# Performance work log

Hardware: AMD Instinct MI355X
Metric: run time of the kernel (lower is better)

## Reference

```python
import jax, jax.numpy as jnp
import numpy as np

B, SQ, SK, D = 8, 2048, 768, 768  # SK must equal D for layer_combine concat to typecheck


def setup_inputs() -> dict:
    key = jax.random.key(0)
    ks = jax.random.split(key, 13)
    s = 0.02
    return {
        "query": jax.random.normal(ks[0], (B, SQ, D), jnp.float32),
        "key_matrix": jax.random.normal(ks[1], (B, SK, D), jnp.float32),
        "value_matrix": jax.random.normal(ks[2], (B, SK, D), jnp.float32),
        "prev_layer": jax.random.normal(ks[3], (SK, D), jnp.float32) * s,
        "attention_mask": jax.random.randint(ks[4], (B, 1, SK), 0, 2, jnp.int32),
        "Wq": jax.random.normal(ks[5], (D, D), jnp.float32) * s,
        "bq": jax.random.normal(ks[6], (D,), jnp.float32) * s,
        "Wk": jax.random.normal(ks[7], (D, D), jnp.float32) * s,
        "bk": jax.random.normal(ks[8], (D,), jnp.float32) * s,
        "Wv": jax.random.normal(ks[9], (D, D), jnp.float32) * s,
        "bv": jax.random.normal(ks[10], (D,), jnp.float32) * s,
        "Wc": jax.random.normal(ks[11], (D, 2 * D), jnp.float32) * s,
        "bc": jax.random.normal(ks[12], (D,), jnp.float32) * s,
    }


def reference(query, key_matrix, value_matrix, prev_layer, attention_mask,
              Wq, bq, Wk, bk, Wv, bv, Wc, bc):
    # Linear projections (torch Linear: x @ W.T + b)
    Q = query @ Wq.T + bq                      # [B, SQ, D]
    K = key_matrix @ Wk.T + bk                 # [B, SK, D]
    V = value_matrix @ Wv.T + bv               # computed but unused when prev_layer given (faithful)
    scale = 1.0 / np.sqrt(D).astype(np.float32)
    scores = jnp.einsum('bqd,bkd->bqk', Q, K) * scale  # [B, SQ, SK]
    scores = jnp.where(attention_mask == 0, jnp.float32(-1e9), scores)
    # prev-layer integration: matmul + concat + linear combine
    layer_attn = scores @ prev_layer           # [B, SQ, D]
    combined = jnp.concatenate([scores, layer_attn], axis=-1)  # [B, SQ, 2D]
    out = combined @ Wc.T + bc                 # [B, SQ, D]
    return out
```

## Files before the change

### kernel.cpp

```cpp
#include <hip/hip_runtime.h>
#include <hip/hip_bf16.h>


typedef __attribute__((ext_vector_type(8))) short short8;
typedef __attribute__((ext_vector_type(4))) float f32x4;

#define SCALE 0.03608439182435161f

__device__ inline unsigned short f2bf(float x) {
  unsigned int u = __builtin_bit_cast(unsigned int, x);
  u = (u + 0x7fffu + ((u >> 16) & 1u)) >> 16;
  return (unsigned short)u;
}
__device__ inline float bf2f(unsigned short h) {
  return __builtin_bit_cast(float, ((unsigned int)h) << 16);
}

__global__ void k_cvt8(const float* __restrict__ s, unsigned short* __restrict__ d, int n8) {
  int i = blockIdx.x * 256 + threadIdx.x;
  if (i >= n8) return;
  const float4* s4 = reinterpret_cast<const float4*>(s);
  float4 v0 = s4[2 * i], v1 = s4[2 * i + 1];
  ushort4* d4 = reinterpret_cast<ushort4*>(d);
  d4[2 * i]     = make_ushort4(f2bf(v0.x), f2bf(v0.y), f2bf(v0.z), f2bf(v0.w));
  d4[2 * i + 1] = make_ushort4(f2bf(v1.x), f2bf(v1.y), f2bf(v1.z), f2bf(v1.w));
}

__global__ void k_prep(const float* __restrict__ prev, const float* __restrict__ Wc,
                       unsigned short* __restrict__ prev_bf,
                       unsigned short* __restrict__ Wc2_bf) {
  int g = blockIdx.x;
  int region = g / 576;
  int idx = (g - region * 576) * 256 + threadIdx.x;
  float4 v;
  unsigned short* dst;
  if (region == 0) { v = reinterpret_cast<const float4*>(prev)[idx]; dst = prev_bf; }
  else {
    int r = idx / 192, c4 = (idx - r * 192) * 4;
    v = *reinterpret_cast<const float4*>(Wc + (long long)r * 1536 + 768 + c4);
    dst = Wc2_bf;
  }
  reinterpret_cast<ushort4*>(dst)[idx] = make_ushort4(f2bf(v.x), f2bf(v.y), f2bf(v.z), f2bf(v.w));
}

__global__ void k_tcvt(const float* __restrict__ Wq, const float* __restrict__ Wk,
                       const float* __restrict__ key, const int* __restrict__ mask,
                       unsigned short* __restrict__ WqT, unsigned short* __restrict__ WkT,
                       unsigned short* __restrict__ keyzT) {
  __shared__ float t[64][65];
  int z = blockIdx.z;
  const float* src;
  unsigned short* dst;
  const int* mb = nullptr;
  if (z == 0) { src = Wq; dst = WqT; }
  else if (z == 1) { src = Wk; dst = WkT; }
  else {
    int b = z - 2;
    src = key + (long long)b * 589824;
    dst = keyzT + (long long)b * 589824;
    mb = mask + b * 768;
  }
  int bx = blockIdx.x * 64, by = blockIdx.y * 64;
  int tx = threadIdx.x & 63, ty = threadIdx.x >> 6;
  #pragma unroll
  for (int i = 0; i < 64; i += 4) {
    float v = src[(long long)(by + ty + i) * 768 + bx + tx];
    if (mb) v = mb[by + ty + i] ? v : 0.0f;
    t[ty + i][tx] = v;
  }
  __syncthreads();
  #pragma unroll
  for (int i = 0; i < 64; i += 4)
    dst[(long long)(bx + ty + i) * 768 + by + tx] = f2bf(t[tx][ty + i]);
}

__global__ void k_sums(const unsigned short* __restrict__ WqT,
                       const unsigned short* __restrict__ WkT,
                       const float* __restrict__ bk, const float* __restrict__ bq,
                       const float* __restrict__ Mt, const int* __restrict__ mask,
                       float* __restrict__ u, float* __restrict__ w3,
                       float* __restrict__ s1, float* __restrict__ sm0) {
  int gw = blockIdx.x * 4 + (threadIdx.x >> 6);
  int lane = threadIdx.x & 63;
  if (gw < 1536) {
    const unsigned short* wrow = (gw < 768) ? (WqT + (long long)gw * 768)
                                            : (WkT + (long long)(gw - 768) * 768);
    const float* vec = (gw < 768) ? bk : bq;
    float s = 0.f;
    for (int j = lane; j < 768; j += 64) s += bf2f(wrow[j]) * vec[j];
    #pragma unroll
    for (int off = 32; off > 0; off >>= 1) s += __shfl_down(s, off, 64);
    if (lane == 0) { if (gw < 768) u[gw] = s; else w3[gw - 768] = s; }
  } else {
    int g2 = gw - 1536;
    int b = g2 / 768, d2 = g2 - b * 768;
    if (b >= 8) return;
    const int* mb = mask + b * 768;
    const float* mrow = Mt + (long long)d2 * 768;
    float a1 = 0.f, a0 = 0.f;
    for (int k = lane; k < 768; k += 64) {
      float v = mrow[k];
      if (mb[k]) a1 += v; else a0 += v;
    }
    #pragma unroll
    for (int off = 32; off > 0; off >>= 1) {
      a1 += __shfl_down(a1, off, 64);
      a0 += __shfl_down(a0, off, 64);
    }
    if (lane == 0) { s1[g2] = a1; sm0[g2] = a0; }
  }
}

__global__ void k_row(const unsigned short* __restrict__ Tt, const float* __restrict__ w3,
                      const float* __restrict__ s1, const float* __restrict__ sm0,
                      const float* __restrict__ bq, const float* __restrict__ bk,
                      const float* __restrict__ bc, float* __restrict__ row) {
  int gw = blockIdx.x * 4 + (threadIdx.x >> 6);
  int lane = threadIdx.x & 63;
  int b = gw / 768, d2 = gw - b * 768;
  if (b >= 8) return;
  const unsigned short* trow = Tt + ((long long)b * 768 + d2) * 768;
  float st = 0.f, sbb = 0.f;
  for (int j = lane; j < 768; j += 64) {
    st += bf2f(trow[j]) * w3[j];
    sbb += bq[j] * bk[j];
  }
  #pragma unroll
  for (int off = 32; off > 0; off >>= 1) {
    st += __shfl_down(st, off, 64);
    sbb += __shfl_down(sbb, off, 64);
  }
  if (lane == 0)
    row[gw] = bc[d2] - 1e9f * sm0[gw] + SCALE * (st + sbb * s1[gw]);
}

__device__ inline void xcd_swz(int& bx, int& by, int& bz) {
  const int gx = gridDim.x, gy = gridDim.y;
  const int nwg = gx * gy * (int)gridDim.z;
  int lin = blockIdx.x + gx * (blockIdx.y + gy * blockIdx.z);
  int qq = nwg >> 3, rr = nwg & 7, xcd = lin & 7, loc = lin >> 3;
  int swz = (xcd < rr ? xcd * (qq + 1) : rr * (qq + 1) + (xcd - rr) * qq) + loc;
  bz = swz / (gx * gy);
  int rem = swz - bz * gx * gy;
  by = rem / gx;
  bx = rem - by * gx;
}

__device__ inline void nt64_core(const unsigned short* Ab, int lda,
                                 const unsigned short* Bb, int ldb,
                                 int m0, int n0, int tid, f32x4 (&acc)[2][2],
                                 char* As, char* Bs) {
  const int w = tid >> 6, lane = tid & 63;
  const int wr = w >> 1, wc = w & 1;
  const int fr = lane & 15, fq = lane >> 4;
  for (int kt = 0; kt < 768; kt += 64) {
    __syncthreads();
    #pragma unroll
    for (int t = 0; t < 2; ++t) {
      int g = t * 256 + tid;
      int row = g >> 3, s = g & 7;
      int sg = (s - row) & 7;
      const unsigned short* ga = Ab + (long long)(m0 + row) * lda + kt + sg * 8;
      __builtin_amdgcn_global_load_lds(
          (const __attribute__((address_space(1))) void*)ga,
          (__attribute__((address_space(3))) void*)(As + g * 16), 16, 0, 0);
    }
    #pragma unroll
    for (int t = 0; t < 2; ++t) {
      int g = t * 256 + tid;
      int row = g >> 3, s = g & 7;
      int sg = (s - row) & 7;
      const unsigned short* gb = Bb + (long long)(n0 + row) * ldb + kt + sg * 8;
      __builtin_amdgcn_global_load_lds(
          (const __attribute__((address_space(1))) void*)gb,
          (__attribute__((address_space(3))) void*)(Bs + g * 16), 16, 0, 0);
    }
    __syncthreads();
    #pragma unroll
    for (int kk = 0; kk < 2; ++kk) {
      short8 af[2], bfr[2];
      #pragma unroll
      for (int i = 0; i < 2; ++i) {
        int r = wr * 32 + i * 16 + fr;
        af[i] = *reinterpret_cast<const short8*>(As + r * 128 + (((kk * 4 + fq) + r) & 7) * 16);
      }
      #pragma unroll
      for (int j = 0; j < 2; ++j) {
        int r = wc * 32 + j * 16 + fr;
        bfr[j] = *reinterpret_cast<const short8*>(Bs + r * 128 + (((kk * 4 + fq) + r) & 7) * 16);
      }
      #pragma unroll
      for (int i = 0; i < 2; ++i)
        #pragma unroll
        for (int j = 0; j < 2; ++j)
          acc[i][j] = __builtin_amdgcn_mfma_f32_16x16x32_bf16(af[i], bfr[j], acc[i][j], 0, 0, 0);
    }
  }
}

__global__ __launch_bounds__(256) void gemm_g1w2(
    const unsigned short* __restrict__ Wc2_bf, const unsigned short* __restrict__ prev_bf,
    const unsigned short* __restrict__ WqT_bf, const unsigned short* __restrict__ WkT_bf,
    const float* __restrict__ Wc, float* __restrict__ Mt_f,
    unsigned short* __restrict__ Mt_bf, unsigned short* __restrict__ W2_bf)
{
  __shared__ __align__(16) char As[64 * 128];
  __shared__ __align__(16) char Bs[64 * 128];
  int bx, by, bz;
  xcd_swz(bx, by, bz);
  const int m0 = by * 64, n0 = bx * 64;
  const unsigned short* A = bz ? WqT_bf : Wc2_bf;
  const unsigned short* B = bz ? WkT_bf : prev_bf;
  const int tid = threadIdx.x;
  f32x4 acc[2][2] = {};
  nt64_core(A, 768, B, 768, m0, n0, tid, acc, As, Bs);

  const int w = tid >> 6, lane = tid & 63;
  const int wr = w >> 1, wc = w & 1;
  const int fr = lane & 15, fq = lane >> 4;
  #pragma unroll
  for (int i = 0; i < 2; ++i)
    #pragma unroll
    for (int j = 0; j < 2; ++j)
      #pragma unroll
      for (int r = 0; r < 4; ++r) {
        int row = m0 + wr * 32 + i * 16 + fq * 4 + r;
        int col = n0 + wc * 32 + j * 16 + fr;
        float v = acc[i][j][r];
        if (bz == 0) {
          v += Wc[(long long)row * 1536 + col];
          Mt_f[(long long)row * 768 + col] = v;
          Mt_bf[(long long)row * 768 + col] = f2bf(v);
        } else {
          W2_bf[(long long)row * 768 + col] = f2bf(v);
        }
      }
}

template <int MODE>
__global__ __launch_bounds__(256) void gemm_nt(
    const unsigned short* __restrict__ A, long long aStr,
    const unsigned short* __restrict__ B, long long bStr,
    unsigned short* __restrict__ Cbf, long long cStr,
    const float* __restrict__ aux, const float* __restrict__ aux2)
{
  __shared__ __align__(16) char As[64 * 128];
  __shared__ __align__(16) char Bs[64 * 128];
  int bx, by, bz;
  xcd_swz(bx, by, bz);
  const int b = bz;
  const int m0 = by * 64, n0 = bx * 64;
  const int tid = threadIdx.x;
  f32x4 acc[2][2] = {};
  nt64_core(A + (long long)b * aStr, 768, B + (long long)b * bStr, 768,
            m0, n0, tid, acc, As, Bs);

  const int w = tid >> 6, lane = tid & 63;
  const int wr = w >> 1, wc = w & 1;
  const int fr = lane & 15, fq = lane >> 4;
  #pragma unroll
  for (int i = 0; i < 2; ++i)
    #pragma unroll
    for (int j = 0; j < 2; ++j)
      #pragma unroll
      for (int r = 0; r < 4; ++r) {
        int row = m0 + wr * 32 + i * 16 + fq * 4 + r;
        int col = n0 + wc * 32 + j * 16 + fr;
        float v = acc[i][j][r];
        if constexpr (MODE == 5) v += aux[b * 768 + row] * aux2[col];
        Cbf[(long long)b * cStr + (long long)row * 768 + col] = f2bf(v);
      }
}

__global__ __launch_bounds__(512, 1) void g5_pipe(
    const unsigned short* __restrict__ A,
    const unsigned short* __restrict__ B,
    float* __restrict__ C, const float* __restrict__ rowv)
{
  __shared__ __align__(16) char As[3][256 * 128];
  __shared__ __align__(16) char Bs[2][192 * 128];

  int lin = blockIdx.x + 4 * (blockIdx.y + 8 * blockIdx.z);
  int swz = (lin & 7) * 32 + (lin >> 3);
  int bz = swz >> 5;
  int rem = swz & 31;
  int by = rem >> 2, bx = rem & 3;

  const int b = bz;
  const int m0 = by * 256, n0 = bx * 192;
  const unsigned short* Ab = A + (long long)b * 1572864;
  const unsigned short* Bb = B + (long long)b * 589824;

  const int tid = threadIdx.x;
  const int w = tid >> 6, lane = tid & 63;
  const int wr = w >> 2, wn = w & 3;
  const int fr = lane & 15, fq = lane >> 4;

  f32x4 acc[8][3] = {};

  auto stageA = [&](int buf, int kt) {
    #pragma unroll
    for (int s = 0; s < 4; ++s) {
      int g = s * 512 + tid;
      int row = g >> 3, slot = g & 7;
      int sg = (slot - row) & 7;
      const unsigned short* ga = Ab + (long long)(m0 + row) * 768 + kt + sg * 8;
      __builtin_amdgcn_global_load_lds(
          (const __attribute__((address_space(1))) void*)ga,
          (__attribute__((address_space(3))) void*)(&As[buf][0] + g * 16), 16, 0, 0);
    }
  };
  auto stageB = [&](int buf, int kt) {
    #pragma unroll
    for (int s = 0; s < 3; ++s) {
      int g = s * 512 + tid;
      int row = g >> 3, slot = g & 7;
      int sg = (slot - row) & 7;
      const unsigned short* gb = Bb + (long long)(n0 + row) * 768 + kt + sg * 8;
      __builtin_amdgcn_global_load_lds(
          (const __attribute__((address_space(1))) void*)gb,
          (__attribute__((address_space(3))) void*)(&Bs[buf][0] + g * 16), 16, 0, 0);
    }
  };

  stageA(0, 0);
  stageB(0, 0);
  stageA(1, 64);
  asm volatile("s_waitcnt vmcnt(4)" ::: "memory");
  __builtin_amdgcn_s_barrier();

  for (int t = 0; t < 12; ++t) {
    const char* as = &As[t % 3][0];
    const char* bs = &Bs[t & 1][0];

    if (t < 11) stageB((t + 1) & 1, (t + 1) * 64);
    if (t < 10) stageA((t + 2) % 3, (t + 2) * 64);

    #pragma unroll
    for (int kk = 0; kk < 2; ++kk) {
      short8 a[8], bb[3];
      #pragma unroll
      for (int i = 0; i < 8; ++i) {
        int r = wr * 128 + i * 16 + fr;
        a[i] = *reinterpret_cast<const short8*>(as + r * 128 + (((kk * 4 + fq) + r) & 7) * 16);
      }
      #pragma unroll
      for (int j = 0; j < 3; ++j) {
        int r = wn * 48 + j * 16 + fr;
        bb[j] = *reinterpret_cast<const short8*>(bs + r * 128 + (((kk * 4 + fq) + r) & 7) * 16);
      }
      __builtin_amdgcn_s_setprio(1);
      #pragma unroll
      for (int i = 0; i < 8; ++i)
        #pragma unroll
        for (int j = 0; j < 3; ++j)
          acc[i][j] = __builtin_amdgcn_mfma_f32_16x16x32_bf16(a[i], bb[j], acc[i][j], 0, 0, 0);
      __builtin_amdgcn_s_setprio(0);
    }

    if (t < 10)       asm volatile("s_waitcnt vmcnt(4)" ::: "memory");
    else if (t == 10) asm volatile("s_waitcnt vmcnt(0)" ::: "memory");
    __builtin_amdgcn_s_barrier();
  }

  const long long ob = (long long)b * 1572864;
  #pragma unroll
  for (int i = 0; i < 8; ++i)
    #pragma unroll
    for (int j = 0; j < 3; ++j)
      #pragma unroll
      for (int r = 0; r < 4; ++r) {
        int row = m0 + wr * 128 + i * 16 + fq * 4 + r;
        int col = n0 + wn * 48 + j * 16 + fr;
        C[ob + (long long)row * 768 + col] = acc[i][j][r] * SCALE + rowv[b * 768 + col];
      }
}

extern "C" void kernel_launch(void* const* d_in, const int* in_sizes, int n_in,
                              void* d_out, int out_size, void* d_ws, size_t ws_size,
                              hipStream_t stream)
{
  const float* query = (const float*)d_in[0];
  const float* key   = (const float*)d_in[1];
  const float* prev  = (const float*)d_in[3];
  const int*   mask  = (const int*)d_in[4];
  const float* Wq    = (const float*)d_in[5];
  const float* bq    = (const float*)d_in[6];
  const float* Wk    = (const float*)d_in[7];
  const float* bk    = (const float*)d_in[8];
  const float* Wc    = (const float*)d_in[11];
  const float* bc    = (const float*)d_in[12];
  float* out = (float*)d_out;

  char* p = (char*)d_ws;
  size_t off = 0;
  auto alloc = [&](size_t bytes) {
    char* r = p + off;
    off += (bytes + 255) & ~(size_t)255;
    return r;
  };
  unsigned short* query_bf = (unsigned short*)alloc(12582912ull * 2);
  unsigned short* keyzT_bf = (unsigned short*)alloc(4718592ull * 2);
  unsigned short* WqT_bf   = (unsigned short*)alloc(589824ull * 2);
  unsigned short* WkT_bf   = (unsigned short*)alloc(589824ull * 2);
  unsigned short* prev_bf  = (unsigned short*)alloc(589824ull * 2);
  unsigned short* Wc2_bf   = (unsigned short*)alloc(589824ull * 2);
  float*          Mt_f     = (float*)alloc(589824ull * 4);
  unsigned short* Mt_bf    = (unsigned short*)alloc(589824ull * 2);
  unsigned short* W2_bf    = (unsigned short*)alloc(589824ull * 2);
  unsigned short* Tt_bf    = (unsigned short*)alloc(4718592ull * 2);
  unsigned short* Pt_bf    = (unsigned short*)alloc(4718592ull * 2);
  float*          s1f      = (float*)alloc(6144ull * 4);
  float*          sm0f     = (float*)alloc(6144ull * 4);
  float*          uv       = (float*)alloc(768ull * 4);
  float*          w3v      = (float*)alloc(768ull * 4);
  float*          rowv     = (float*)alloc(6144ull * 4);
  (void)ws_size; (void)in_sizes; (void)n_in; (void)out_size;

  k_cvt8<<<dim3(6144), dim3(256), 0, stream>>>(query, query_bf, 1572864);
  k_tcvt<<<dim3(12, 12, 10), dim3(256), 0, stream>>>(Wq, Wk, key, mask,
                                                     WqT_bf, WkT_bf, keyzT_bf);
  k_prep<<<dim3(1152), dim3(256), 0, stream>>>(prev, Wc, prev_bf, Wc2_bf);

  gemm_g1w2<<<dim3(12, 12, 2), dim3(256), 0, stream>>>(
      Wc2_bf, prev_bf, WqT_bf, WkT_bf, Wc, Mt_f, Mt_bf, W2_bf);
  k_sums<<<dim3(1920), dim3(256), 0, stream>>>(WqT_bf, WkT_bf, bk, bq, Mt_f, mask,
                                               uv, w3v, s1f, sm0f);
  gemm_nt<2><<<dim3(12, 12, 8), dim3(256), 0, stream>>>(
      Mt_bf, 0ll, keyzT_bf, 589824ll, Tt_bf, 589824ll,
      (const float*)nullptr, (const float*)nullptr);
  gemm_nt<5><<<dim3(12, 12, 8), dim3(256), 0, stream>>>(
      Tt_bf, 589824ll, W2_bf, 0ll, Pt_bf, 589824ll, s1f, uv);
  k_row<<<dim3(1536), dim3(256), 0, stream>>>(Tt_bf, w3v, s1f, sm0f, bq, bk, bc, rowv);
  g5_pipe<<<dim3(4, 8, 8), dim3(512), 0, stream>>>(query_bf, Pt_bf, out, rowv);
}
```

Baseline: 110.4 us.

## Fuse prep kernels and fold reductions into pipelined larger-tile GEMMs

After: 250.8 us. +127.2%, slower.

```diff
diff --git a/kernel.cpp b/kernel.cpp
--- a/kernel.cpp
+++ b/kernel.cpp
@@ -16,122 +16,70 @@
   return __builtin_bit_cast(float, ((unsigned int)h) << 16);
 }
 
-__global__ void k_cvt8(const float* __restrict__ s, unsigned short* __restrict__ d, int n8) {
-  int i = blockIdx.x * 256 + threadIdx.x;
-  if (i >= n8) return;
-  const float4* s4 = reinterpret_cast<const float4*>(s);
-  float4 v0 = s4[2 * i], v1 = s4[2 * i + 1];
-  ushort4* d4 = reinterpret_cast<ushort4*>(d);
-  d4[2 * i]     = make_ushort4(f2bf(v0.x), f2bf(v0.y), f2bf(v0.z), f2bf(v0.w));
-  d4[2 * i + 1] = make_ushort4(f2bf(v1.x), f2bf(v1.y), f2bf(v1.z), f2bf(v1.w));
-}
-
-__global__ void k_prep(const float* __restrict__ prev, const float* __restrict__ Wc,
-                       unsigned short* __restrict__ prev_bf,
-                       unsigned short* __restrict__ Wc2_bf) {
-  int g = blockIdx.x;
-  int region = g / 576;
-  int idx = (g - region * 576) * 256 + threadIdx.x;
-  float4 v;
-  unsigned short* dst;
-  if (region == 0) { v = reinterpret_cast<const float4*>(prev)[idx]; dst = prev_bf; }
-  else {
-    int r = idx / 192, c4 = (idx - r * 192) * 4;
-    v = *reinterpret_cast<const float4*>(Wc + (long long)r * 1536 + 768 + c4);
-    dst = Wc2_bf;
-  }
-  reinterpret_cast<ushort4*>(dst)[idx] = make_ushort4(f2bf(v.x), f2bf(v.y), f2bf(v.z), f2bf(v.w));
-}
-
-__global__ void k_tcvt(const float* __restrict__ Wq, const float* __restrict__ Wk,
-                       const float* __restrict__ key, const int* __restrict__ mask,
-                       unsigned short* __restrict__ WqT, unsigned short* __restrict__ WkT,
-                       unsigned short* __restrict__ keyzT) {
+__global__ void k_prep_all(
+    const float* __restrict__ Wq, const float* __restrict__ Wk,
+    const float* __restrict__ key, const int* __restrict__ mask,
+    const float* __restrict__ prev, const float* __restrict__ Wc,
+    const float* __restrict__ query,
+    unsigned short* __restrict__ WqT, unsigned short* __restrict__ WkT,
+    unsigned short* __restrict__ keyzT, unsigned short* __restrict__ prev_bf,
+    unsigned short* __restrict__ Wc2_bf, unsigned short* __restrict__ query_bf)
+{
   __shared__ float t[64][65];
-  int z = blockIdx.z;
-  const float* src;
-  unsigned short* dst;
-  const int* mb = nullptr;
-  if (z == 0) { src = Wq; dst = WqT; }
-  else if (z == 1) { src = Wk; dst = WkT; }
-  else {
-    int b = z - 2;
-    src = key + (long long)b * 589824;
-    dst = keyzT + (long long)b * 589824;
-    mb = mask + b * 768;
-  }
-  int bx = blockIdx.x * 64, by = blockIdx.y * 64;
-  int tx = threadIdx.x & 63, ty = threadIdx.x >> 6;
+  const int z = blockIdx.z;
+  const int tid = threadIdx.x;
+  if (z < 10) {
+    const float* src;
+    unsigned short* dst;
+    const int* mb = nullptr;
+    if (z == 0) { src = Wq; dst = WqT; }
+    else if (z == 1) { src = Wk; dst = WkT; }
+    else {
+      int b = z - 2;
+      src = key + (long long)b * 589824;
+      dst = keyzT + (long long)b * 589824;
+      mb = mask + b * 768;
+    }
+    int bx = blockIdx.x * 64, by = blockIdx.y * 64;
+    int tx = tid & 63, ty = tid >> 6;
+    #pragma unroll
+    for (int i = 0; i < 64; i += 4) {
+      float v = src[(long long)(by + ty + i) * 768 + bx + tx];
+      if (mb) v = mb[by + ty + i] ? v : 0.0f;
+      t[ty + i][tx] = v;
+    }
+    __syncthreads();
+    #pragma unroll
+    for (int i = 0; i < 64; i += 4)
+      dst[(long long)(bx + ty + i) * 768 + by + tx] = f2bf(t[tx][ty + i]);
+    return;
+  }
+  const int r = tid >> 2, c0 = (tid & 3) * 16;
+  const float* sr;
+  unsigned short* dr;
+  if (z == 10) {
+    int row = blockIdx.y * 64 + r, col = blockIdx.x * 64 + c0;
+    sr = prev + (long long)row * 768 + col;
+    dr = prev_bf + (long long)row * 768 + col;
+  } else if (z == 11) {
+    int row = blockIdx.y * 64 + r, col = blockIdx.x * 64 + c0;
+    sr = Wc + (long long)row * 1536 + 768 + col;
+    dr = Wc2_bf + (long long)row * 768 + col;
+  } else {
+    int tz = (z - 12) * 144 + blockIdx.y * 12 + blockIdx.x;
+    if (tz >= 3072) return;
+    int b = tz / 384, rmn = tz - b * 384;
+    int rt = rmn / 12, ct = rmn - rt * 12;
+    long long base = (long long)b * 1572864 + (long long)(rt * 64 + r) * 768 + ct * 64 + c0;
+    sr = query + base;
+    dr = query_bf + base;
+  }
   #pragma unroll
-  for (int i = 0; i < 64; i += 4) {
-    float v = src[(long long)(by + ty + i) * 768 + bx + tx];
-    if (mb) v = mb[by + ty + i] ? v : 0.0f;
-    t[ty + i][tx] = v;
-  }
-  __syncthreads();
-  #pragma unroll
-  for (int i = 0; i < 64; i += 4)
-    dst[(long long)(bx + ty + i) * 768 + by + tx] = f2bf(t[tx][ty + i]);
-}
-
-__global__ void k_sums(const unsigned short* __restrict__ WqT,
-                       const unsigned short* __restrict__ WkT,
-                       const float* __restrict__ bk, const float* __restrict__ bq,
-                       const float* __restrict__ Mt, const int* __restrict__ mask,
-                       float* __restrict__ u, float* __restrict__ w3,
-                       float* __restrict__ s1, float* __restrict__ sm0) {
-  int gw = blockIdx.x * 4 + (threadIdx.x >> 6);
-  int lane = threadIdx.x & 63;
-  if (gw < 1536) {
-    const unsigned short* wrow = (gw < 768) ? (WqT + (long long)gw * 768)
-                                            : (WkT + (long long)(gw - 768) * 768);
-    const float* vec = (gw < 768) ? bk : bq;
-    float s = 0.f;
-    for (int j = lane; j < 768; j += 64) s += bf2f(wrow[j]) * vec[j];
-    #pragma unroll
-    for (int off = 32; off > 0; off >>= 1) s += __shfl_down(s, off, 64);
-    if (lane == 0) { if (gw < 768) u[gw] = s; else w3[gw - 768] = s; }
-  } else {
-    int g2 = gw - 1536;
-    int b = g2 / 768, d2 = g2 - b * 768;
-    if (b >= 8) return;
-    const int* mb = mask + b * 768;
-    const float* mrow = Mt + (long long)d2 * 768;
-    float a1 = 0.f, a0 = 0.f;
-    for (int k = lane; k < 768; k += 64) {
-      float v = mrow[k];
-      if (mb[k]) a1 += v; else a0 += v;
-    }
-    #pragma unroll
-    for (int off = 32; off > 0; off >>= 1) {
-      a1 += __shfl_down(a1, off, 64);
-      a0 += __shfl_down(a0, off, 64);
-    }
-    if (lane == 0) { s1[g2] = a1; sm0[g2] = a0; }
-  }
-}
-
-__global__ void k_row(const unsigned short* __restrict__ Tt, const float* __restrict__ w3,
-                      const float* __restrict__ s1, const float* __restrict__ sm0,
-                      const float* __restrict__ bq, const float* __restrict__ bk,
-                      const float* __restrict__ bc, float* __restrict__ row) {
-  int gw = blockIdx.x * 4 + (threadIdx.x >> 6);
-  int lane = threadIdx.x & 63;
-  int b = gw / 768, d2 = gw - b * 768;
-  if (b >= 8) return;
-  const unsigned short* trow = Tt + ((long long)b * 768 + d2) * 768;
-  float st = 0.f, sbb = 0.f;
-  for (int j = lane; j < 768; j += 64) {
-    st += bf2f(trow[j]) * w3[j];
-    sbb += bq[j] * bk[j];
-  }
-  #pragma unroll
-  for (int off = 32; off > 0; off >>= 1) {
-    st += __shfl_down(st, off, 64);
-    sbb += __shfl_down(sbb, off, 64);
-  }
-  if (lane == 0)
-    row[gw] = bc[d2] - 1e9f * sm0[gw] + SCALE * (st + sbb * s1[gw]);
+  for (int q = 0; q < 4; ++q) {
+    float4 v = *reinterpret_cast<const float4*>(sr + q * 4);
+    *reinterpret_cast<ushort4*>(dr + q * 4) =
+        make_ushort4(f2bf(v.x), f2bf(v.y), f2bf(v.z), f2bf(v.w));
+  }
 }
 
 __device__ inline void xcd_swz(int& bx, int& by, int& bz) {
@@ -238,37 +186,170 @@
 }
 
 template <int MODE>
-__global__ __launch_bounds__(256) void gemm_nt(
+__global__ __launch_bounds__(512, 1) void g34_pipe(
     const unsigned short* __restrict__ A, long long aStr,
     const unsigned short* __restrict__ B, long long bStr,
-    unsigned short* __restrict__ Cbf, long long cStr,
-    const float* __restrict__ aux, const float* __restrict__ aux2)
+    unsigned short* __restrict__ C,
+    const float* __restrict__ s1, const float* __restrict__ uv,
+    const unsigned short* __restrict__ WqT, const unsigned short* __restrict__ WkT,
+    const float* __restrict__ bk, const float* __restrict__ bq,
+    const float* __restrict__ Mt_f, const int* __restrict__ mask,
+    const unsigned short* __restrict__ Tt, const float* __restrict__ w3,
+    const float* __restrict__ sm0, const float* __restrict__ bc,
+    float* __restrict__ o_u, float* __restrict__ o_w3,
+    float* __restrict__ o_s1, float* __restrict__ o_sm0, float* __restrict__ o_row)
 {
-  __shared__ __align__(16) char As[64 * 128];
-  __shared__ __align__(16) char Bs[64 * 128];
-  int bx, by, bz;
-  xcd_swz(bx, by, bz);
+  __shared__ __align__(16) char As[3][96 * 128];
+  __shared__ __align__(16) char Bs[2][192 * 128];
+
+  int lin = blockIdx.x + 4 * (blockIdx.y + 8 * blockIdx.z);
+  int swz = (lin & 7) * 36 + (lin >> 3);
+  int bz = swz >> 5;
+  int rem = swz & 31;
+  int by = rem >> 2, bx = rem & 3;
+
+  const int tid = threadIdx.x;
+  const int wv = tid >> 6, lane = tid & 63;
+
+  if (bz == 8) {
+    int gw0 = (swz - 256) * 8 + wv;
+    if constexpr (MODE == 3) {
+      for (int unit = gw0; unit < 7680; unit += 256) {
+        if (unit < 1536) {
+          const unsigned short* wrow = (unit < 768) ? (WqT + (long long)unit * 768)
+                                                    : (WkT + (long long)(unit - 768) * 768);
+          const float* vec = (unit < 768) ? bk : bq;
+          float s = 0.f;
+          for (int j = lane; j < 768; j += 64) s += bf2f(wrow[j]) * vec[j];
+          #pragma unroll
+          for (int off = 32; off > 0; off >>= 1) s += __shfl_down(s, off, 64);
+          if (lane == 0) { if (unit < 768) o_u[unit] = s; else o_w3[unit - 768] = s; }
+        } else {
+          int g2 = unit - 1536;
+          int b = g2 / 768, d2 = g2 - b * 768;
+          const int* mb = mask + b * 768;
+          const float* mrow = Mt_f + (long long)d2 * 768;
+          float a1 = 0.f, a0 = 0.f;
+          for (int k = lane; k < 768; k += 64) {
+            float v = mrow[k];
+            if (mb[k]) a1 += v; else a0 += v;
+          }
+          #pragma unroll
+          for (int off = 32; off > 0; off >>= 1) {
+            a1 += __shfl_down(a1, off, 64);
+            a0 += __shfl_down(a0, off, 64);
+          }
+          if (lane == 0) { o_s1[g2] = a1; o_sm0[g2] = a0; }
+        }
+      }
+    } else {
+      for (int unit = gw0; unit < 6144; unit += 256) {
+        int b = unit / 768, d2 = unit - b * 768;
+        const unsigned short* trow = Tt + ((long long)b * 768 + d2) * 768;
+        float st = 0.f, sbb = 0.f;
+        for (int j = lane; j < 768; j += 64) {
+          st += bf2f(trow[j]) * w3[j];
+          sbb += bq[j] * bk[j];
+        }
+        #pragma unroll
+        for (int off = 32; off > 0; off >>= 1) {
+          st += __shfl_down(st, off, 64);
+          sbb += __shfl_down(sbb, off, 64);
+        }
+        if (lane == 0)
+          o_row[unit] = bc[d2] - 1e9f * sm0[unit] + SCALE * (st + sbb * s1[unit]);
+      }
+    }
+    return;
+  }
+
   const int b = bz;
-  const int m0 = by * 64, n0 = bx * 64;
-  const int tid = threadIdx.x;
-  f32x4 acc[2][2] = {};
-  nt64_core(A + (long long)b * aStr, 768, B + (long long)b * bStr, 768,
-            m0, n0, tid, acc, As, Bs);
-
-  const int w = tid >> 6, lane = tid & 63;
-  const int wr = w >> 1, wc = w & 1;
+  const int m0 = by * 96, n0 = bx * 192;
+  const unsigned short* Ab = A + (long long)b * aStr;
+  const unsigned short* Bb = B + (long long)b * bStr;
+  const int wr = wv >> 2, wn = wv & 3;
   const int fr = lane & 15, fq = lane >> 4;
+
+  f32x4 acc[3][3] = {};
+
+  auto stageA = [&](int buf, int kt) {
+    #pragma unroll
+    for (int s = 0; s < 2; ++s) {
+      int g = s * 512 + tid;
+      if (g < 768) {
+        int row = g >> 3, slot = g & 7;
+        int sg = (slot - row) & 7;
+        const unsigned short* ga = Ab + (long long)(m0 + row) * 768 + kt + sg * 8;
+        __builtin_amdgcn_global_load_lds(
+            (const __attribute__((address_space(1))) void*)ga,
+            (__attribute__((address_space(3))) void*)(&As[buf][0] + g * 16), 16, 0, 0);
+      }
+    }
+  };
+  auto stageB = [&](int buf, int kt) {
+    #pragma unroll
+    for (int s = 0; s < 3; ++s) {
+      int g = s * 512 + tid;
+      int row = g >> 3, slot = g & 7;
+      int sg = (slot - row) & 7;
+      const unsigned short* gb = Bb + (long long)(n0 + row) * 768 + kt + sg * 8;
+      __builtin_amdgcn_global_load_lds(
+          (const __attribute__((address_space(1))) void*)gb,
+          (__attribute__((address_space(3))) void*)(&Bs[buf][0] + g * 16), 16, 0, 0);
+    }
+  };
+
+  stageA(0, 0);
+  stageB(0, 0);
+  stageA(1, 64);
+  asm volatile("s_waitcnt vmcnt(1)" ::: "memory");
+  __builtin_amdgcn_s_barrier();
+
+  for (int t = 0; t < 12; ++t) {
+    const char* as = &As[t % 3][0];
+    const char* bs = &Bs[t & 1][0];
+
+    if (t < 11) stageB((t + 1) & 1, (t + 1) * 64);
+    if (t < 10) stageA((t + 2) % 3, (t + 2) * 64);
+
+    #pragma unroll
+    for (int kk = 0; kk < 2; ++kk) {
+      short8 a[3], bb[3];
+      #pragma unroll
+      for (int i = 0; i < 3; ++i) {
+        int r = wr * 48 + i * 16 + fr;
+        a[i] = *reinterpret_cast<const short8*>(as + r * 128 + (((kk * 4 + fq) + r) & 7) * 16);
+      }
+      #pragma unroll
+      for (int j = 0; j < 3; ++j) {
+        int r = wn * 48 + j * 16 + fr;
+        bb[j] = *reinterpret_cast<const short8*>(bs + r * 128 + (((kk * 4 + fq) + r) & 7) * 16);
+      }
+      __builtin_amdgcn_s_setprio(1);
+      #pragma unroll
+      for (int i = 0; i < 3; ++i)
+        #pragma unroll
+        for (int j = 0; j < 3; ++j)
+          acc[i][j] = __builtin_amdgcn_mfma_f32_16x16x32_bf16(a[i], bb[j], acc[i][j], 0, 0, 0);
+      __builtin_amdgcn_s_setprio(0);
+    }
+
+    if (t < 10)       asm volatile("s_waitcnt vmcnt(1)" ::: "memory");
+    else if (t == 10) asm volatile("s_waitcnt vmcnt(0)" ::: "memory");
+    __builtin_amdgcn_s_barrier();
+  }
+
   #pragma unroll
-  for (int i = 0; i < 2; ++i)
-    #pragma unroll
-    for (int j = 0; j < 2; ++j)
+  for (int i = 0; i < 3; ++i)
+    #pragma unroll
+    for (int j = 0; j < 3; ++j)
       #pragma unroll
       for (int r = 0; r < 4; ++r) {
-        int row = m0 + wr * 32 + i * 16 + fq * 4 + r;
-        int col = n0 + wc * 32 + j * 16 + fr;
+        int row = m0 + wr * 48 + i * 16 + fq * 4 + r;
+        int col = n0 + wn * 48 + j * 16 + fr;
         float v = acc[i][j][r];
-        if constexpr (MODE == 5) v += aux[b * 768 + row] * aux2[col];
-        Cbf[(long long)b * cStr + (long long)row * 768 + col] = f2bf(v);
+        if constexpr (MODE == 4) v += s1[b * 768 + row] * uv[col];
+        C[(long long)b * 589824 + (long long)row * 768 + col] = f2bf(v);
       }
 }
 
@@ -417,20 +498,24 @@
   float*          rowv     = (float*)alloc(6144ull * 4);
   (void)ws_size; (void)in_sizes; (void)n_in; (void)out_size;
 
-  k_cvt8<<<dim3(6144), dim3(256), 0, stream>>>(query, query_bf, 1572864);
-  k_tcvt<<<dim3(12, 12, 10), dim3(256), 0, stream>>>(Wq, Wk, key, mask,
-                                                     WqT_bf, WkT_bf, keyzT_bf);
-  k_prep<<<dim3(1152), dim3(256), 0, stream>>>(prev, Wc, prev_bf, Wc2_bf);
-
+  k_prep_all<<<dim3(12, 12, 34), dim3(256), 0, stream>>>(
+      Wq, Wk, key, mask, prev, Wc, query,
+      WqT_bf, WkT_bf, keyzT_bf, prev_bf, Wc2_bf, query_bf);
   gemm_g1w2<<<dim3(12, 12, 2), dim3(256), 0, stream>>>(
       Wc2_bf, prev_bf, WqT_bf, WkT_bf, Wc, Mt_f, Mt_bf, W2_bf);
-  k_sums<<<dim3(1920), dim3(256), 0, stream>>>(WqT_bf, WkT_bf, bk, bq, Mt_f, mask,
-                                               uv, w3v, s1f, sm0f);
-  gemm_nt<2><<<dim3(12, 12, 8), dim3(256), 0, stream>>>(
-      Mt_bf, 0ll, keyzT_bf, 589824ll, Tt_bf, 589824ll,
-      (const float*)nullptr, (const float*)nullptr);
-  gemm_nt<5><<<dim3(12, 12, 8), dim3(256), 0, stream>>>(
-      Tt_bf, 589824ll, W2_bf, 0ll, Pt_bf, 589824ll, s1f, uv);
-  k_row<<<dim3(1536), dim3(256), 0, stream>>>(Tt_bf, w3v, s1f, sm0f, bq, bk, bc, rowv);
+  g34_pipe<3><<<dim3(4, 8, 9), dim3(512), 0, stream>>>(
+      Mt_bf, 0ll, keyzT_bf, 589824ll, Tt_bf,
+      (const float*)nullptr, (const float*)nullptr,
+      WqT_bf, WkT_bf, bk, bq, Mt_f, mask,
+      (const unsigned short*)nullptr, (const float*)nullptr,
+      (const float*)nullptr, (const float*)nullptr,
+      uv, w3v, s1f, sm0f, (float*)nullptr);
+  g34_pipe<4><<<dim3(4, 8, 9), dim3(512), 0, stream>>>(
+      Tt_bf, 589824ll, W2_bf, 0ll, Pt_bf,
+      s1f, uv,
+      (const unsigned short*)nullptr, (const unsigned short*)nullptr, bk, bq,
+      (const float*)nullptr, (const int*)nullptr,
+      Tt_bf, w3v, sm0f, bc,
+      (float*)nullptr, (float*)nullptr, (float*)nullptr, (float*)nullptr, rowv);
   g5_pipe<<<dim3(4, 8, 8), dim3(512), 0, stream>>>(query_bf, Pt_bf, out, rowv);
 }
```
